# Optimization experiments

Measured on AMD Instinct MI355X. Metric: run time of the kernel, lower is better.

## Reference

```python
import jax, jax.numpy as jnp
import numpy as np

N_EMBD = 1024
N_HEAD = 16
SEQ_LEN = 2048
BATCH = 4
ROPE_THETA = 10000.0


def _rope_tables(T, hd, dtype=jnp.float32):
    freqs = 1.0 / (ROPE_THETA ** (jnp.arange(0, hd, 2, dtype=jnp.float32) / hd))
    t = jnp.arange(T, dtype=jnp.float32)
    ang = jnp.outer(t, freqs)  # [T, hd//2]
    return jnp.cos(ang).astype(dtype), jnp.sin(ang).astype(dtype)


def _apply_rope(x, cos, sin):
    # x: [B,H,T,hd]; cos/sin: [T, hd//2]
    hd = x.shape[-1]
    x1, x2 = x[..., : hd // 2], x[..., hd // 2 :]
    c = cos[None, None, : x.shape[2], :]
    s = sin[None, None, : x.shape[2], :]
    return jnp.concatenate([x1 * c - x2 * s, x2 * c + x1 * s], axis=-1)


def _rms_norm(x):
    eps = jnp.finfo(x.dtype).eps
    return x * jax.lax.rsqrt(jnp.mean(jnp.square(x), axis=-1, keepdims=True) + eps)


def setup_inputs() -> dict:
    key = jax.random.key(0)
    k1, k2, k3, k4 = jax.random.split(key, 4)
    C = N_EMBD
    x = jax.random.normal(k1, (BATCH, SEQ_LEN, C), dtype=jnp.float32)
    w_attn = jax.random.normal(k2, (C, 3 * C), dtype=jnp.float32) * (1.0 / np.sqrt(C))
    w_proj = jax.random.normal(k3, (C, C), dtype=jnp.float32) * (1.0 / np.sqrt(C))
    val_embed = jax.random.normal(k4, (SEQ_LEN, C), dtype=jnp.float32) * 0.02
    return {"x": x, "w_attn": w_attn, "w_proj": w_proj, "val_embed": val_embed}


def reference(x, w_attn, w_proj, val_embed):
    B, T, C = x.shape
    H = N_HEAD
    hd = C // H

    qkv = x @ w_attn  # [B,T,3C]
    q, k, v = jnp.split(qkv, 3, axis=-1)
    v = v + val_embed[:T]

    def to_heads(t):
        return t.reshape(B, T, H, hd).transpose(0, 2, 1, 3)  # [B,H,T,hd]

    q, k, v = to_heads(q), to_heads(k), to_heads(v)

    cos, sin = _rope_tables(T, hd, x.dtype)
    q = _rms_norm(_apply_rope(q, cos, sin))
    k = _rms_norm(_apply_rope(k, cos, sin))

    scale = 1.0 / np.sqrt(hd)
    scores = jnp.einsum("bhqd,bhkd->bhqk", q, k) * scale  # [B,H,T,T]
    causal = jnp.tril(jnp.ones((T, T), dtype=bool))
    scores = jnp.where(causal[None, None], scores, jnp.finfo(scores.dtype).min)
    attn = jax.nn.softmax(scores, axis=-1)
    y = jnp.einsum("bhqk,bhkd->bhqd", attn, v)  # [B,H,T,hd]
    y = y.transpose(0, 2, 1, 3).reshape(B, T, C)
    return y @ w_proj
```

## Files before the change

### kernel.cpp

```cpp
#include <hip/hip_runtime.h>
#include <float.h>
#include <math.h>

#define BB 4
#define TT 2048
#define CC 1024
#define HH 16
#define HD 64
#define C3 3072

typedef __bf16 bf16;
typedef __bf16 bf16x8 __attribute__((ext_vector_type(8)));
typedef __bf16 bf16x4 __attribute__((ext_vector_type(4)));
typedef float f32x4 __attribute__((ext_vector_type(4)));
typedef float f32x16 __attribute__((ext_vector_type(16)));
typedef unsigned int uint32x4 __attribute__((ext_vector_type(4)));

#define QSCALE 0.18033688f

__device__ __forceinline__ void gload16(const void* g, void* l) {
    __builtin_amdgcn_global_load_lds(
        (const __attribute__((address_space(1))) void*)g,
        (__attribute__((address_space(3))) void*)l, 16, 0, 0);
}

__global__ __launch_bounds__(256) void rope_table_k(float* __restrict__ tab) {
    int idx = blockIdx.x * 256 + threadIdx.x;
    if (idx >= TT * 32) return;
    int t = idx >> 5;
    int j = idx & 31;
    float freq = powf(10000.0f, -((float)(2 * j)) / 64.0f);
    float ang = (float)t * freq;
    tab[idx] = cosf(ang);
    tab[TT * 32 + idx] = sinf(ang);
}

__global__ __launch_bounds__(256) void cvt_f2b_k(const float* __restrict__ in,
                                                 bf16* __restrict__ out, int n8) {
    int i = blockIdx.x * 256 + threadIdx.x;
    if (i >= n8) return;
    const float4* p = (const float4*)(in + (size_t)i * 8);
    float4 a = p[0], b = p[1];
    bf16x8 o;
    o[0] = (bf16)a.x; o[1] = (bf16)a.y; o[2] = (bf16)a.z; o[3] = (bf16)a.w;
    o[4] = (bf16)b.x; o[5] = (bf16)b.y; o[6] = (bf16)b.z; o[7] = (bf16)b.w;
    *(bf16x8*)(out + (size_t)i * 8) = o;
}

__global__ __launch_bounds__(256) void transW_k(const float* __restrict__ in,
                                                bf16* __restrict__ out, int K, int N) {
    __shared__ bf16 tile[64][72];
    int n0 = blockIdx.x * 64, k0 = blockIdx.y * 64;
    int t = threadIdx.x;
    int r = t >> 2, c4 = (t & 3) * 16;
    const float4* src = (const float4*)(in + (size_t)(k0 + r) * N + n0 + c4);
    #pragma unroll
    for (int j = 0; j < 4; ++j) {
        float4 v = src[j];
        tile[r][c4 + 4 * j + 0] = (bf16)v.x; tile[r][c4 + 4 * j + 1] = (bf16)v.y;
        tile[r][c4 + 4 * j + 2] = (bf16)v.z; tile[r][c4 + 4 * j + 3] = (bf16)v.w;
    }
    __syncthreads();
    bf16x8 o0, o1;
    #pragma unroll
    for (int j = 0; j < 8; ++j) o0[j] = tile[c4 + j][r];
    #pragma unroll
    for (int j = 0; j < 8; ++j) o1[j] = tile[c4 + 8 + j][r];
    *(bf16x8*)(out + (size_t)(n0 + r) * K + k0 + c4) = o0;
    *(bf16x8*)(out + (size_t)(n0 + r) * K + k0 + c4 + 8) = o1;
}

__global__ __launch_bounds__(512) void gemm256_k(const bf16* __restrict__ A,
                                                 const bf16* __restrict__ BT,
                                                 bf16* __restrict__ Qh,
                                                 bf16* __restrict__ Kh,
                                                 bf16* __restrict__ Vh,
                                                 int M, int N, int K) {
    extern __shared__ bf16 smem[];
    const int tid = threadIdx.x;
    const int w = tid >> 6, lane = tid & 63;
    const int wm = w >> 2, wn = w & 3;
    const int nwg = (int)gridDim.x;
    const int cpx = nwg >> 3;
    const int flat = (int)blockIdx.x;
    const int wg = (flat & 7) * cpx + (flat >> 3);
    const int gx = N >> 8;
    const int n0 = (wg % gx) * 256;
    const int m0 = (wg / gx) * 256;

    const int srow = lane >> 3;
    const int schunk = (lane & 7) ^ srow;
    const int xorL = (lane & 7) << 3;
    const int KT = K >> 6;

    f32x4 acc[8][4];
    #pragma unroll
    for (int i = 0; i < 8; ++i)
        #pragma unroll
        for (int j = 0; j < 4; ++j) acc[i][j] = {0.f, 0.f, 0.f, 0.f};

    {
        bf16* Al = smem;
        bf16* Bl = smem + 16384;
        #pragma unroll
        for (int i = 0; i < 4; ++i) {
            int row = i * 64 + w * 8;
            gload16(A + (size_t)(m0 + row + srow) * K + schunk * 8, Al + row * 64);
            gload16(BT + (size_t)(n0 + row + srow) * K + schunk * 8, Bl + row * 64);
        }
    }
    __syncthreads();

    for (int kt = 0; kt < KT; ++kt) {
        const int buf = kt & 1;
        if (kt + 1 < KT) {
            bf16* Al = smem + (buf ^ 1) * 32768;
            bf16* Bl = Al + 16384;
            const int k0 = (kt + 1) * 64;
            #pragma unroll
            for (int i = 0; i < 4; ++i) {
                int row = i * 64 + w * 8;
                gload16(A + (size_t)(m0 + row + srow) * K + k0 + schunk * 8,
                        Al + row * 64);
                gload16(BT + (size_t)(n0 + row + srow) * K + k0 + schunk * 8,
                        Bl + row * 64);
            }
        }
        const bf16* Al = smem + buf * 32768;
        const bf16* Bl = Al + 16384;
        #pragma unroll
        for (int kh = 0; kh < 2; ++kh) {
            const int off = (kh * 32 + (lane >> 4) * 8) ^ xorL;
            bf16x8 aF[8], bF[4];
            #pragma unroll
            for (int i = 0; i < 8; ++i)
                aF[i] = *(const bf16x8*)&Al[(wm * 128 + i * 16 + (lane & 15)) * 64 + off];
            #pragma unroll
            for (int j = 0; j < 4; ++j)
                bF[j] = *(const bf16x8*)&Bl[(wn * 64 + j * 16 + (lane & 15)) * 64 + off];
            __builtin_amdgcn_s_setprio(1);
            #pragma unroll
            for (int i = 0; i < 8; ++i)
                #pragma unroll
                for (int j = 0; j < 4; ++j)
                    acc[i][j] = __builtin_amdgcn_mfma_f32_16x16x32_bf16(
                        aF[i], bF[j], acc[i][j], 0, 0, 0);
            __builtin_amdgcn_s_setprio(0);
        }
        __syncthreads();
    }

    const int ncb = n0 + wn * 64;
    const int region = ncb >> 10;
    const int h = (ncb & 1023) >> 6;
    bf16* dst = (region == 0) ? Qh : ((region == 1) ? Kh : Vh);
    #pragma unroll
    for (int i = 0; i < 8; ++i)
        #pragma unroll
        for (int r = 0; r < 4; ++r) {
            int m = m0 + wm * 128 + i * 16 + 4 * (lane >> 4) + r;
            int b = m >> 11, t = m & (TT - 1);
            size_t rb = ((size_t)(b * HH + h) * TT + t) * HD;
            #pragma unroll
            for (int j = 0; j < 4; ++j)
                dst[rb + j * 16 + (lane & 15)] = (bf16)acc[i][j][r];
        }
}

__global__ __launch_bounds__(256) void gemm_bt_k(const bf16* __restrict__ A,
                                                 const bf16* __restrict__ BT,
                                                 float* __restrict__ C,
                                                 int M, int N, int K) {
    __shared__ bf16 Al[128 * 64];
    __shared__ bf16 Bl[128 * 64];
    const int tid = threadIdx.x;
    const int w = tid >> 6, lane = tid & 63;
    const int m0 = blockIdx.y * 128, n0 = blockIdx.x * 128;
    const int wrow = (w >> 1) * 64, wcol = (w & 1) * 64;
    const int srow = lane >> 3;
    const int selem = (((lane & 7) ^ srow) << 3);
    const int xorL = (lane & 7) << 3;

    const f32x4 fz = {0.f, 0.f, 0.f, 0.f};
    f32x4 acc[4][4];
    #pragma unroll
    for (int i = 0; i < 4; ++i)
        #pragma unroll
        for (int j = 0; j < 4; ++j) acc[i][j] = fz;

    for (int k0 = 0; k0 < K; k0 += 64) {
        __syncthreads();
        #pragma unroll
        for (int jj = 0; jj < 4; ++jj) {
            int c = w * 4 + jj;
            int row = c * 8 + srow;
            gload16(A + (size_t)(m0 + row) * K + k0 + selem, &Al[c * 512]);
            gload16(BT + (size_t)(n0 + row) * K + k0 + selem, &Bl[c * 512]);
        }
        __syncthreads();
        #pragma unroll
        for (int kh = 0; kh < 2; ++kh) {
            const int off = (kh * 32 + (lane >> 4) * 8) ^ xorL;
            bf16x8 aF[4], bF[4];
            #pragma unroll
            for (int i = 0; i < 4; ++i) {
                aF[i] = *(const bf16x8*)&Al[(wrow + i * 16 + (lane & 15)) * 64 + off];
                bF[i] = *(const bf16x8*)&Bl[(wcol + i * 16 + (lane & 15)) * 64 + off];
            }
            #pragma unroll
            for (int i = 0; i < 4; ++i)
                #pragma unroll
                for (int j = 0; j < 4; ++j)
                    acc[i][j] = __builtin_amdgcn_mfma_f32_16x16x32_bf16(
                        aF[i], bF[j], acc[i][j], 0, 0, 0);
        }
    }

    #pragma unroll
    for (int i = 0; i < 4; ++i)
        #pragma unroll
        for (int r = 0; r < 4; ++r) {
            size_t rowm = (size_t)(m0 + wrow + i * 16 + 4 * (lane >> 4) + r);
            #pragma unroll
            for (int j = 0; j < 4; ++j)
                C[rowm * N + n0 + wcol + j * 16 + (lane & 15)] = acc[i][j][r];
        }
}

__global__ __launch_bounds__(256) void rope_rms_k(bf16* __restrict__ Qh,
                                                  bf16* __restrict__ Kh,
                                                  const bf16* __restrict__ Vh,
                                                  bf16* __restrict__ Vt,
                                                  const float* __restrict__ emb,
                                                  const float* __restrict__ tab) {
    __shared__ bf16 tile[64][72];
    const int t0 = blockIdx.x * 64;
    const int bh = blockIdx.y;
    const int h = bh & (HH - 1);
    const int w = threadIdx.x >> 6, lane = threadIdx.x & 63;
    const int j = lane & 31;
    #pragma unroll 4
    for (int i = 0; i < 16; ++i) {
        const int tl = w * 16 + i;
        const int t = t0 + tl;
        const size_t base = ((size_t)bh * TT + t) * HD + lane;
        const float cs = tab[t * 32 + j];
        const float sn = tab[TT * 32 + t * 32 + j];
        float q = (float)Qh[base], k = (float)Kh[base], v = (float)Vh[base];
        float qp = __shfl_xor(q, 32, 64), kp = __shfl_xor(k, 32, 64);
        float rq = (lane < 32) ? q * cs - qp * sn : q * cs + qp * sn;
        float rk = (lane < 32) ? k * cs - kp * sn : k * cs + kp * sn;
        float sq = rq * rq, sk = rk * rk;
        #pragma unroll
        for (int off = 1; off < 64; off <<= 1) {
            sq += __shfl_xor(sq, off, 64);
            sk += __shfl_xor(sk, off, 64);
        }
        rq *= rsqrtf(sq * (1.0f / 64.0f) + 1.1920929e-07f);
        rk *= rsqrtf(sk * (1.0f / 64.0f) + 1.1920929e-07f);
        Qh[base] = (bf16)(rq * QSCALE);
        Kh[base] = (bf16)rk;
        tile[tl][lane] = (bf16)(v + emb[(size_t)t * CC + h * HD + lane]);
    }
    __syncthreads();
    const int tt = threadIdx.x;
    const int r = tt >> 2, c4 = (tt & 3) * 16;
    bf16x8 o0, o1;
    #pragma unroll
    for (int jj = 0; jj < 8; ++jj) o0[jj] = tile[c4 + jj][r];
    #pragma unroll
    for (int jj = 0; jj < 8; ++jj) o1[jj] = tile[c4 + 8 + jj][r];
    bf16* out = Vt + (size_t)bh * HD * TT;
    *(bf16x8*)(out + (size_t)r * TT + t0 + c4) = o0;
    *(bf16x8*)(out + (size_t)r * TT + t0 + c4 + 8) = o1;
}

__global__ __launch_bounds__(512) void attn_k(const bf16* __restrict__ Qh,
                                              const bf16* __restrict__ Kh,
                                              const bf16* __restrict__ Vt,
                                              bf16* __restrict__ Y) {
    const int flat = (int)blockIdx.y * 8 + (int)blockIdx.x;
    const int slot = flat >> 3;
    const int bh = (flat & 7) * 8 + (slot & 7);
    const int qb = 7 - (slot >> 3);
    const int b = bh >> 4, h = bh & 15;
    const int tid = threadIdx.x, w = tid >> 6, lane = tid & 63;
    const int hi = lane >> 5, q31 = lane & 31;
    const int wq0 = qb * 256 + w * 32;
    const int qg = wq0 + q31;
    const int xr = q31 & 7;

    __shared__ bf16 Kl[3][64 * 64];
    __shared__ bf16 Vl[3][64 * 64];

    const bf16* Kbase = Kh + (size_t)bh * TT * HD;
    const bf16* Vbase = Vt + (size_t)bh * HD * TT;

    bf16x8 qF[4];
    {
        const bf16* qp = Qh + (size_t)bh * TT * HD + (size_t)qg * HD + hi * 8;
        #pragma unroll
        for (int ds = 0; ds < 4; ++ds) qF[ds] = *(const bf16x8*)(qp + ds * 16);
    }

    f32x16 accY[2];
    #pragma unroll
    for (int i = 0; i < 16; ++i) { accY[0][i] = 0.f; accY[1][i] = 0.f; }
    float mR = -INFINITY, lR = 0.f;

    const int srow = lane >> 3;
    const int schunk = (lane & 7) ^ srow;
    const int ktN = 4 * qb + 4;

    {
        int r0 = w * 8 + srow;
        gload16(Kbase + (size_t)r0 * HD + schunk * 8, &Kl[0][w * 512]);
        gload16(Vbase + (size_t)r0 * TT + schunk * 8, &Vl[0][w * 512]);
        gload16(Kbase + (size_t)(64 + r0) * HD + schunk * 8, &Kl[1][w * 512]);
        gload16(Vbase + (size_t)r0 * TT + 64 + schunk * 8, &Vl[1][w * 512]);
    }
    asm volatile("s_waitcnt vmcnt(2)" ::: "memory");
    __builtin_amdgcn_s_barrier();
    __builtin_amdgcn_sched_barrier(0);

    int bufC = 0, bufS = 2;
    for (int kt = 0; kt < ktN; ++kt) {
        if (kt + 2 < ktN) {
            int trow = (kt + 2) * 64 + w * 8 + srow;
            int drow = w * 8 + srow;
            gload16(Kbase + (size_t)trow * HD + schunk * 8, &Kl[bufS][w * 512]);
            gload16(Vbase + (size_t)drow * TT + (kt + 2) * 64 + schunk * 8,
                    &Vl[bufS][w * 512]);
        }
        if (kt * 64 <= wq0 + 31) {
            const bf16* KL = &Kl[bufC][0];
            const bf16* VL = &Vl[bufC][0];
            f32x16 sa[2];
            #pragma unroll
            for (int i = 0; i < 16; ++i) { sa[0][i] = 0.f; sa[1][i] = 0.f; }
            __builtin_amdgcn_s_setprio(1);
            #pragma unroll
            for (int ds = 0; ds < 4; ++ds) {
                int cc = ds * 2 + hi;
                bf16x8 k0 = *(const bf16x8*)&KL[q31 * 64 + ((cc ^ xr) * 8)];
                bf16x8 k1 = *(const bf16x8*)&KL[(32 + q31) * 64 + ((cc ^ xr) * 8)];
                sa[0] = __builtin_amdgcn_mfma_f32_32x32x16_bf16(k0, qF[ds], sa[0], 0, 0, 0);
                sa[1] = __builtin_amdgcn_mfma_f32_32x32x16_bf16(k1, qF[ds], sa[1], 0, 0, 0);
            }
            __builtin_amdgcn_s_setprio(0);
            if (kt * 64 + 63 > wq0) {
                #pragma unroll
                for (int kb = 0; kb < 2; ++kb)
                    #pragma unroll
                    for (int r = 0; r < 16; ++r) {
                        int k = kt * 64 + kb * 32 + (r & 3) + 8 * (r >> 2) + 4 * hi;
                        if (k > qg) sa[kb][r] = -1e30f;
                    }
            }
            float mx = -1e30f;
            #pragma unroll
            for (int r = 0; r < 16; ++r) {
                mx = fmaxf(mx, sa[0][r]);
                mx = fmaxf(mx, sa[1][r]);
            }
            mx = fmaxf(mx, __shfl_xor(mx, 32, 64));
            if (!__all(mx - mR <= 12.0f)) {
                float mnew = fmaxf(mR, mx);
                float alpha = __builtin_amdgcn_exp2f(mR - mnew);
                #pragma unroll
                for (int i = 0; i < 16; ++i) { accY[0][i] *= alpha; accY[1][i] *= alpha; }
                lR *= alpha;
                mR = mnew;
            }
            float sum = 0.f;
            #pragma unroll
            for (int kb = 0; kb < 2; ++kb)
                #pragma unroll
                for (int r = 0; r < 16; ++r) {
                    float p = __builtin_amdgcn_exp2f(sa[kb][r] - mR);
                    sa[kb][r] = p;
                    sum += p;
                }
            sum += __shfl_xor(sum, 32, 64);
            lR += sum;
            unsigned int wds[2][8];
            #pragma unroll
            for (int kb = 0; kb < 2; ++kb)
                #pragma unroll
                for (int jj = 0; jj < 8; ++jj) {
                    bf16x8 tmp;
                    tmp[0] = (bf16)sa[kb][2 * jj];
                    tmp[1] = (bf16)sa[kb][2 * jj + 1];
                    wds[kb][jj] = *(unsigned int*)&tmp;
                }
            bf16x8 pF[4];
            #pragma unroll
            for (int ks = 0; ks < 4; ++ks) {
                const int kb = ks >> 1, s = ks & 1;
                unsigned int w0 = wds[kb][4 * s + 0], w1 = wds[kb][4 * s + 1];
                unsigned int w2 = wds[kb][4 * s + 2], w3 = wds[kb][4 * s + 3];
                unsigned int t0 = hi ? w0 : w2, t1 = hi ? w1 : w3;
                unsigned int r0 = (unsigned int)__shfl_xor((int)t0, 32, 64);
                unsigned int r1 = (unsigned int)__shfl_xor((int)t1, 32, 64);
                uint32x4 fw;
                fw[0] = hi ? r0 : w0; fw[1] = hi ? r1 : w1;
                fw[2] = hi ? w2 : r0; fw[3] = hi ? w3 : r1;
                pF[ks] = *(bf16x8*)&fw;
            }
            __builtin_amdgcn_s_setprio(1);
            #pragma unroll
            for (int cd = 0; cd < 2; ++cd) {
                const int rowD = cd * 32 + q31;
                #pragma unroll
                for (int ks = 0; ks < 4; ++ks) {
                    int cc = ks * 2 + hi;
                    bf16x8 vA = *(const bf16x8*)&VL[rowD * 64 + ((cc ^ xr) * 8)];
                    accY[cd] = __builtin_amdgcn_mfma_f32_32x32x16_bf16(
                        vA, pF[ks], accY[cd], 0, 0, 0);
                }
            }
            __builtin_amdgcn_s_setprio(0);
        }
        if (kt + 1 < ktN) {
            if (kt + 2 < ktN) {
                asm volatile("s_waitcnt vmcnt(2)" ::: "memory");
            } else {
                asm volatile("s_waitcnt vmcnt(0)" ::: "memory");
            }
            __builtin_amdgcn_s_barrier();
            __builtin_amdgcn_sched_barrier(0);
        }
        bufC = (bufC == 2) ? 0 : bufC + 1;
        bufS = (bufS == 2) ? 0 : bufS + 1;
    }

    float inv = 1.0f / lR;
    bf16* yp = Y + ((size_t)(b * TT + qg)) * CC + h * HD;
    #pragma unroll
    for (int cd = 0; cd < 2; ++cd)
        #pragma unroll
        for (int g = 0; g < 4; ++g) {
            int d0 = cd * 32 + 8 * g + 4 * hi;
            bf16x4 o;
            o[0] = (bf16)(accY[cd][4 * g + 0] * inv);
            o[1] = (bf16)(accY[cd][4 * g + 1] * inv);
            o[2] = (bf16)(accY[cd][4 * g + 2] * inv);
            o[3] = (bf16)(accY[cd][4 * g + 3] * inv);
            *(bf16x4*)(yp + d0) = o;
        }
}

extern "C" void kernel_launch(void* const* d_in, const int* in_sizes, int n_in,
                              void* d_out, int out_size, void* d_ws, size_t ws_size,
                              hipStream_t stream) {
    const float* x         = (const float*)d_in[0];
    const float* w_attn    = (const float*)d_in[1];
    const float* w_proj    = (const float*)d_in[2];
    const float* val_embed = (const float*)d_in[3];
    float* out = (float*)d_out;

    bf16* xb  = (bf16*)d_ws;
    bf16* waT = xb + (size_t)8192 * 1024;
    bf16* wpT = waT + (size_t)3072 * 1024;
    bf16* Qh  = wpT + (size_t)1024 * 1024;
    bf16* Kh  = Qh + (size_t)64 * 2048 * 64;
    bf16* Vh  = Kh + (size_t)64 * 2048 * 64;
    bf16* Vt  = Vh + (size_t)64 * 2048 * 64;
    bf16* Yb  = Vt + (size_t)64 * 2048 * 64;
    float* tab = (float*)(Yb + (size_t)64 * 2048 * 64);

    hipFuncSetAttribute((const void*)gemm256_k,
                        hipFuncAttributeMaxDynamicSharedMemorySize, 131072);

    rope_table_k<<<dim3((TT * 32 + 255) / 256), dim3(256), 0, stream>>>(tab);
    cvt_f2b_k<<<dim3(8192 * 1024 / 8 / 256), dim3(256), 0, stream>>>(x, xb, 8192 * 1024 / 8);
    transW_k<<<dim3(3072 / 64, 1024 / 64), dim3(256), 0, stream>>>(w_attn, waT, 1024, 3072);
    transW_k<<<dim3(1024 / 64, 1024 / 64), dim3(256), 0, stream>>>(w_proj, wpT, 1024, 1024);
    gemm256_k<<<dim3((8192 / 256) * (3072 / 256)), dim3(512), 131072, stream>>>(
        xb, waT, Qh, Kh, Vh, 8192, 3072, 1024);
    rope_rms_k<<<dim3(TT / 64, BB * HH), dim3(256), 0, stream>>>(
        Qh, Kh, Vh, Vt, val_embed, tab);
    attn_k<<<dim3(8, BB * HH), dim3(512), 0, stream>>>(Qh, Kh, Vt, Yb);
    gemm_bt_k<<<dim3(1024 / 128, 8192 / 128), dim3(256), 0, stream>>>(
        Yb, wpT, out, 8192, 1024, 1024);
}
```

Baseline: 194.6 us.

## Triple-buffer QKV GEMM with 256x128 tiles and fuse value-embedding add

The QKV GEMM moves from 256x256 tiles with double buffering to 256x128 tiles with a three-stage LDS pipeline. It uses explicit vmcnt waits and raw barriers so two k-tiles stay in flight, and it doubles the grid. The val_embed add moves into the GEMM epilogue for V columns, so rope_rms_k no longer reads V plus the embedding. The attention softmax max and sum loops are split into two independent accumulators for more ILP. Smaller tiles lower arithmetic intensity and need more LDS, which may limit occupancy, in exchange for better latency hiding and load balance.

```diff
diff --git a/kernel.cpp b/kernel.cpp
--- a/kernel.cpp
+++ b/kernel.cpp
@@ -70,100 +70,115 @@
     *(bf16x8*)(out + (size_t)(n0 + r) * K + k0 + c4 + 8) = o1;
 }
 
-__global__ __launch_bounds__(512) void gemm256_k(const bf16* __restrict__ A,
-                                                 const bf16* __restrict__ BT,
-                                                 bf16* __restrict__ Qh,
-                                                 bf16* __restrict__ Kh,
-                                                 bf16* __restrict__ Vh,
-                                                 int M, int N, int K) {
+__global__ __launch_bounds__(512) void gemm_qkv_k(const bf16* __restrict__ A,
+                                                  const bf16* __restrict__ BT,
+                                                  bf16* __restrict__ Qh,
+                                                  bf16* __restrict__ Kh,
+                                                  bf16* __restrict__ Vh,
+                                                  const float* __restrict__ emb) {
     extern __shared__ bf16 smem[];
+    const int N = 3072, K = 1024;
     const int tid = threadIdx.x;
     const int w = tid >> 6, lane = tid & 63;
-    const int wm = w >> 2, wn = w & 3;
+    const int wm = w >> 1, wn = w & 1;
     const int nwg = (int)gridDim.x;
     const int cpx = nwg >> 3;
     const int flat = (int)blockIdx.x;
     const int wg = (flat & 7) * cpx + (flat >> 3);
-    const int gx = N >> 8;
-    const int n0 = (wg % gx) * 256;
+    const int gx = N / 128;
+    const int n0 = (wg % gx) * 128;
     const int m0 = (wg / gx) * 256;
-
     const int srow = lane >> 3;
     const int schunk = (lane & 7) ^ srow;
     const int xorL = (lane & 7) << 3;
-    const int KT = K >> 6;
-
-    f32x4 acc[8][4];
-    #pragma unroll
-    for (int i = 0; i < 8; ++i)
+    const int KT = K / 64;
+
+    f32x4 acc[4][4];
+    #pragma unroll
+    for (int i = 0; i < 4; ++i)
         #pragma unroll
         for (int j = 0; j < 4; ++j) acc[i][j] = {0.f, 0.f, 0.f, 0.f};
 
-    {
-        bf16* Al = smem;
-        bf16* Bl = smem + 16384;
-        #pragma unroll
-        for (int i = 0; i < 4; ++i) {
-            int row = i * 64 + w * 8;
-            gload16(A + (size_t)(m0 + row + srow) * K + schunk * 8, Al + row * 64);
-            gload16(BT + (size_t)(n0 + row + srow) * K + schunk * 8, Bl + row * 64);
-        }
-    }
-    __syncthreads();
+    auto stage = [&](int kt, int buf) {
+        bf16* Al = smem + buf * 24576;
+        bf16* Bl = Al + 16384;
+        const int k0 = kt * 64;
+        #pragma unroll
+        for (int rnd = 0; rnd < 4; ++rnd) {
+            int row = rnd * 64 + w * 8;
+            gload16(A + (size_t)(m0 + row + srow) * K + k0 + schunk * 8,
+                    Al + row * 64);
+        }
+        #pragma unroll
+        for (int rnd = 0; rnd < 2; ++rnd) {
+            int row = rnd * 64 + w * 8;
+            gload16(BT + (size_t)(n0 + row + srow) * K + k0 + schunk * 8,
+                    Bl + row * 64);
+        }
+    };
+
+    stage(0, 0);
+    stage(1, 1);
+    asm volatile("s_waitcnt vmcnt(6)" ::: "memory");
+    __builtin_amdgcn_s_barrier();
+    __builtin_amdgcn_sched_barrier(0);
 
     for (int kt = 0; kt < KT; ++kt) {
-        const int buf = kt & 1;
-        if (kt + 1 < KT) {
-            bf16* Al = smem + (buf ^ 1) * 32768;
-            bf16* Bl = Al + 16384;
-            const int k0 = (kt + 1) * 64;
-            #pragma unroll
-            for (int i = 0; i < 4; ++i) {
-                int row = i * 64 + w * 8;
-                gload16(A + (size_t)(m0 + row + srow) * K + k0 + schunk * 8,
-                        Al + row * 64);
-                gload16(BT + (size_t)(n0 + row + srow) * K + k0 + schunk * 8,
-                        Bl + row * 64);
-            }
-        }
-        const bf16* Al = smem + buf * 32768;
+        if (kt + 2 < KT) stage(kt + 2, (kt + 2) % 3);
+        const bf16* Al = smem + (kt % 3) * 24576;
         const bf16* Bl = Al + 16384;
         #pragma unroll
         for (int kh = 0; kh < 2; ++kh) {
             const int off = (kh * 32 + (lane >> 4) * 8) ^ xorL;
-            bf16x8 aF[8], bF[4];
-            #pragma unroll
-            for (int i = 0; i < 8; ++i)
-                aF[i] = *(const bf16x8*)&Al[(wm * 128 + i * 16 + (lane & 15)) * 64 + off];
+            bf16x8 aF[4], bF[4];
+            #pragma unroll
+            for (int i = 0; i < 4; ++i)
+                aF[i] = *(const bf16x8*)&Al[(wm * 64 + i * 16 + (lane & 15)) * 64 + off];
             #pragma unroll
             for (int j = 0; j < 4; ++j)
                 bF[j] = *(const bf16x8*)&Bl[(wn * 64 + j * 16 + (lane & 15)) * 64 + off];
             __builtin_amdgcn_s_setprio(1);
             #pragma unroll
-            for (int i = 0; i < 8; ++i)
+            for (int i = 0; i < 4; ++i)
                 #pragma unroll
                 for (int j = 0; j < 4; ++j)
                     acc[i][j] = __builtin_amdgcn_mfma_f32_16x16x32_bf16(
                         aF[i], bF[j], acc[i][j], 0, 0, 0);
             __builtin_amdgcn_s_setprio(0);
         }
-        __syncthreads();
+        if (kt + 1 < KT) {
+            if (kt + 2 < KT) {
+                asm volatile("s_waitcnt vmcnt(6)" ::: "memory");
+            } else {
+                asm volatile("s_waitcnt vmcnt(0)" ::: "memory");
+            }
+            __builtin_amdgcn_s_barrier();
+            __builtin_amdgcn_sched_barrier(0);
+        }
     }
 
     const int ncb = n0 + wn * 64;
     const int region = ncb >> 10;
     const int h = (ncb & 1023) >> 6;
     bf16* dst = (region == 0) ? Qh : ((region == 1) ? Kh : Vh);
-    #pragma unroll
-    for (int i = 0; i < 8; ++i)
+    const float* ebase = emb + h * 64;
+    #pragma unroll
+    for (int i = 0; i < 4; ++i)
         #pragma unroll
         for (int r = 0; r < 4; ++r) {
-            int m = m0 + wm * 128 + i * 16 + 4 * (lane >> 4) + r;
+            int m = m0 + wm * 64 + i * 16 + 4 * (lane >> 4) + r;
             int b = m >> 11, t = m & (TT - 1);
             size_t rb = ((size_t)(b * HH + h) * TT + t) * HD;
-            #pragma unroll
-            for (int j = 0; j < 4; ++j)
-                dst[rb + j * 16 + (lane & 15)] = (bf16)acc[i][j][r];
+            if (region == 2) {
+                #pragma unroll
+                for (int j = 0; j < 4; ++j)
+                    dst[rb + j * 16 + (lane & 15)] =
+                        (bf16)(acc[i][j][r] + ebase[(size_t)t * CC + j * 16 + (lane & 15)]);
+            } else {
+                #pragma unroll
+                for (int j = 0; j < 4; ++j)
+                    dst[rb + j * 16 + (lane & 15)] = (bf16)acc[i][j][r];
+            }
         }
 }
 
@@ -231,12 +246,10 @@
                                                   bf16* __restrict__ Kh,
                                                   const bf16* __restrict__ Vh,
                                                   bf16* __restrict__ Vt,
-                                                  const float* __restrict__ emb,
                                                   const float* __restrict__ tab) {
     __shared__ bf16 tile[64][72];
     const int t0 = blockIdx.x * 64;
     const int bh = blockIdx.y;
-    const int h = bh & (HH - 1);
     const int w = threadIdx.x >> 6, lane = threadIdx.x & 63;
     const int j = lane & 31;
     #pragma unroll 4
@@ -246,7 +259,7 @@
         const size_t base = ((size_t)bh * TT + t) * HD + lane;
         const float cs = tab[t * 32 + j];
         const float sn = tab[TT * 32 + t * 32 + j];
-        float q = (float)Qh[base], k = (float)Kh[base], v = (float)Vh[base];
+        float q = (float)Qh[base], k = (float)Kh[base];
         float qp = __shfl_xor(q, 32, 64), kp = __shfl_xor(k, 32, 64);
         float rq = (lane < 32) ? q * cs - qp * sn : q * cs + qp * sn;
         float rk = (lane < 32) ? k * cs - kp * sn : k * cs + kp * sn;
@@ -260,7 +273,7 @@
         rk *= rsqrtf(sk * (1.0f / 64.0f) + 1.1920929e-07f);
         Qh[base] = (bf16)(rq * QSCALE);
         Kh[base] = (bf16)rk;
-        tile[tl][lane] = (bf16)(v + emb[(size_t)t * CC + h * HD + lane]);
+        tile[tl][lane] = Vh[base];
     }
     __syncthreads();
     const int tt = threadIdx.x;
@@ -359,10 +372,8 @@
             }
             float mx = -1e30f;
             #pragma unroll
-            for (int r = 0; r < 16; ++r) {
-                mx = fmaxf(mx, sa[0][r]);
-                mx = fmaxf(mx, sa[1][r]);
-            }
+            for (int r = 0; r < 16; ++r)
+                mx = fmaxf(fmaxf(sa[0][r], sa[1][r]), mx);
             mx = fmaxf(mx, __shfl_xor(mx, 32, 64));
             if (!__all(mx - mR <= 12.0f)) {
                 float mnew = fmaxf(mR, mx);
@@ -372,15 +383,15 @@
                 lR *= alpha;
                 mR = mnew;
             }
-            float sum = 0.f;
-            #pragma unroll
-            for (int kb = 0; kb < 2; ++kb)
-                #pragma unroll
-                for (int r = 0; r < 16; ++r) {
-                    float p = __builtin_amdgcn_exp2f(sa[kb][r] - mR);
-                    sa[kb][r] = p;
-                    sum += p;
-                }
+            float sum0 = 0.f, sum1 = 0.f;
+            #pragma unroll
+            for (int r = 0; r < 16; ++r) {
+                float p0 = __builtin_amdgcn_exp2f(sa[0][r] - mR);
+                float p1 = __builtin_amdgcn_exp2f(sa[1][r] - mR);
+                sa[0][r] = p0; sa[1][r] = p1;
+                sum0 += p0; sum1 += p1;
+            }
+            float sum = sum0 + sum1;
             sum += __shfl_xor(sum, 32, 64);
             lR += sum;
             unsigned int wds[2][8];
@@ -469,17 +480,17 @@
     bf16* Yb  = Vt + (size_t)64 * 2048 * 64;
     float* tab = (float*)(Yb + (size_t)64 * 2048 * 64);
 
-    hipFuncSetAttribute((const void*)gemm256_k,
-                        hipFuncAttributeMaxDynamicSharedMemorySize, 131072);
+    hipFuncSetAttribute((const void*)gemm_qkv_k,
+                        hipFuncAttributeMaxDynamicSharedMemorySize, 147456);
 
     rope_table_k<<<dim3((TT * 32 + 255) / 256), dim3(256), 0, stream>>>(tab);
     cvt_f2b_k<<<dim3(8192 * 1024 / 8 / 256), dim3(256), 0, stream>>>(x, xb, 8192 * 1024 / 8);
     transW_k<<<dim3(3072 / 64, 1024 / 64), dim3(256), 0, stream>>>(w_attn, waT, 1024, 3072);
     transW_k<<<dim3(1024 / 64, 1024 / 64), dim3(256), 0, stream>>>(w_proj, wpT, 1024, 1024);
-    gemm256_k<<<dim3((8192 / 256) * (3072 / 256)), dim3(512), 131072, stream>>>(
-        xb, waT, Qh, Kh, Vh, 8192, 3072, 1024);
+    gemm_qkv_k<<<dim3((8192 / 256) * (3072 / 128)), dim3(512), 147456, stream>>>(
+        xb, waT, Qh, Kh, Vh, val_embed);
     rope_rms_k<<<dim3(TT / 64, BB * HH), dim3(256), 0, stream>>>(
-        Qh, Kh, Vh, Vt, val_embed, tab);
+        Qh, Kh, Vh, Vt, tab);
     attn_k<<<dim3(8, BB * HH), dim3(512), 0, stream>>>(Qh, Kh, Vt, Yb);
     gemm_bt_k<<<dim3(1024 / 128, 8192 / 128), dim3(256), 0, stream>>>(
         Yb, wpT, out, 8192, 1024, 1024);
```

Result: slower. 199.6 us (+2.6%).

## Fuse value-embedding add into QKV GEMM epilogue and remap output GEMM blocks per XCD

Applied to the files above, without the earlier changes.

Moves the val_embed addition from the rope/RMS kernel into the QKV GEMM epilogue for the V region, so rope_rms_k copies V directly into the transpose tile. The output projection GEMM switches to a flat 1D grid remapped so each XCD handles a contiguous band of M rows, aiming for better L2 reuse of A tiles. It also restructures the attention softmax max and exp-sum loops into two independent accumulator chains to shorten dependency chains. The epilogue now does uncoalesced-ish fp32 embed loads per element in the GEMM, and the GEMM dimensions become hard-coded constants.

```diff
diff --git a/kernel.cpp b/kernel.cpp
--- a/kernel.cpp
+++ b/kernel.cpp
@@ -75,8 +75,9 @@
                                                  bf16* __restrict__ Qh,
                                                  bf16* __restrict__ Kh,
                                                  bf16* __restrict__ Vh,
-                                                 int M, int N, int K) {
+                                                 const float* __restrict__ emb) {
     extern __shared__ bf16 smem[];
+    const int N = 3072, K = 1024;
     const int tid = threadIdx.x;
     const int w = tid >> 6, lane = tid & 63;
     const int wm = w >> 2, wn = w & 3;
@@ -154,6 +155,7 @@
     const int region = ncb >> 10;
     const int h = (ncb & 1023) >> 6;
     bf16* dst = (region == 0) ? Qh : ((region == 1) ? Kh : Vh);
+    const float* ebase = emb + h * 64;
     #pragma unroll
     for (int i = 0; i < 8; ++i)
         #pragma unroll
@@ -161,9 +163,16 @@
             int m = m0 + wm * 128 + i * 16 + 4 * (lane >> 4) + r;
             int b = m >> 11, t = m & (TT - 1);
             size_t rb = ((size_t)(b * HH + h) * TT + t) * HD;
-            #pragma unroll
-            for (int j = 0; j < 4; ++j)
-                dst[rb + j * 16 + (lane & 15)] = (bf16)acc[i][j][r];
+            if (region == 2) {
+                #pragma unroll
+                for (int j = 0; j < 4; ++j)
+                    dst[rb + j * 16 + (lane & 15)] =
+                        (bf16)(acc[i][j][r] + ebase[(size_t)t * CC + j * 16 + (lane & 15)]);
+            } else {
+                #pragma unroll
+                for (int j = 0; j < 4; ++j)
+                    dst[rb + j * 16 + (lane & 15)] = (bf16)acc[i][j][r];
+            }
         }
 }
 
@@ -175,7 +184,12 @@
     __shared__ bf16 Bl[128 * 64];
     const int tid = threadIdx.x;
     const int w = tid >> 6, lane = tid & 63;
-    const int m0 = blockIdx.y * 128, n0 = blockIdx.x * 128;
+    const int flat = (int)blockIdx.x;
+    const int xcd = flat & 7;
+    const int local = flat >> 3;
+    const int lr = local >> 3, lc = local & 7;
+    const int m0 = (xcd * 8 + lr) * 128;
+    const int n0 = lc * 128;
     const int wrow = (w >> 1) * 64, wcol = (w & 1) * 64;
     const int srow = lane >> 3;
     const int selem = (((lane & 7) ^ srow) << 3);
@@ -231,12 +245,10 @@
                                                   bf16* __restrict__ Kh,
                                                   const bf16* __restrict__ Vh,
                                                   bf16* __restrict__ Vt,
-                                                  const float* __restrict__ emb,
                                                   const float* __restrict__ tab) {
     __shared__ bf16 tile[64][72];
     const int t0 = blockIdx.x * 64;
     const int bh = blockIdx.y;
-    const int h = bh & (HH - 1);
     const int w = threadIdx.x >> 6, lane = threadIdx.x & 63;
     const int j = lane & 31;
     #pragma unroll 4
@@ -246,7 +258,7 @@
         const size_t base = ((size_t)bh * TT + t) * HD + lane;
         const float cs = tab[t * 32 + j];
         const float sn = tab[TT * 32 + t * 32 + j];
-        float q = (float)Qh[base], k = (float)Kh[base], v = (float)Vh[base];
+        float q = (float)Qh[base], k = (float)Kh[base];
         float qp = __shfl_xor(q, 32, 64), kp = __shfl_xor(k, 32, 64);
         float rq = (lane < 32) ? q * cs - qp * sn : q * cs + qp * sn;
         float rk = (lane < 32) ? k * cs - kp * sn : k * cs + kp * sn;
@@ -260,7 +272,7 @@
         rk *= rsqrtf(sk * (1.0f / 64.0f) + 1.1920929e-07f);
         Qh[base] = (bf16)(rq * QSCALE);
         Kh[base] = (bf16)rk;
-        tile[tl][lane] = (bf16)(v + emb[(size_t)t * CC + h * HD + lane]);
+        tile[tl][lane] = Vh[base];
     }
     __syncthreads();
     const int tt = threadIdx.x;
@@ -359,10 +371,8 @@
             }
             float mx = -1e30f;
             #pragma unroll
-            for (int r = 0; r < 16; ++r) {
-                mx = fmaxf(mx, sa[0][r]);
-                mx = fmaxf(mx, sa[1][r]);
-            }
+            for (int r = 0; r < 16; ++r)
+                mx = fmaxf(fmaxf(sa[0][r], sa[1][r]), mx);
             mx = fmaxf(mx, __shfl_xor(mx, 32, 64));
             if (!__all(mx - mR <= 12.0f)) {
                 float mnew = fmaxf(mR, mx);
@@ -372,15 +382,15 @@
                 lR *= alpha;
                 mR = mnew;
             }
-            float sum = 0.f;
-            #pragma unroll
-            for (int kb = 0; kb < 2; ++kb)
-                #pragma unroll
-                for (int r = 0; r < 16; ++r) {
-                    float p = __builtin_amdgcn_exp2f(sa[kb][r] - mR);
-                    sa[kb][r] = p;
-                    sum += p;
-                }
+            float sum0 = 0.f, sum1 = 0.f;
+            #pragma unroll
+            for (int r = 0; r < 16; ++r) {
+                float p0 = __builtin_amdgcn_exp2f(sa[0][r] - mR);
+                float p1 = __builtin_amdgcn_exp2f(sa[1][r] - mR);
+                sa[0][r] = p0; sa[1][r] = p1;
+                sum0 += p0; sum1 += p1;
+            }
+            float sum = sum0 + sum1;
             sum += __shfl_xor(sum, 32, 64);
             lR += sum;
             unsigned int wds[2][8];
@@ -477,10 +487,10 @@
     transW_k<<<dim3(3072 / 64, 1024 / 64), dim3(256), 0, stream>>>(w_attn, waT, 1024, 3072);
     transW_k<<<dim3(1024 / 64, 1024 / 64), dim3(256), 0, stream>>>(w_proj, wpT, 1024, 1024);
     gemm256_k<<<dim3((8192 / 256) * (3072 / 256)), dim3(512), 131072, stream>>>(
-        xb, waT, Qh, Kh, Vh, 8192, 3072, 1024);
+        xb, waT, Qh, Kh, Vh, val_embed);
     rope_rms_k<<<dim3(TT / 64, BB * HH), dim3(256), 0, stream>>>(
-        Qh, Kh, Vh, Vt, val_embed, tab);
+        Qh, Kh, Vh, Vt, tab);
     attn_k<<<dim3(8, BB * HH), dim3(512), 0, stream>>>(Qh, Kh, Vt, Yb);
-    gemm_bt_k<<<dim3(1024 / 128, 8192 / 128), dim3(256), 0, stream>>>(
+    gemm_bt_k<<<dim3(512), dim3(256), 0, stream>>>(
         Yb, wpT, out, 8192, 1024, 1024);
 }
```

Result: slower. 200.7 us (+3.1%).
